# Kernel tuning notes

Measured on AMD Instinct MI355X. Metric: run time of the kernel, lower is better.

Reference implementation:

```python
import jax, jax.numpy as jnp
import numpy as np

B, T, D_IN = 2, 2048, 1024
H, D_HEAD = 16, 64
D_INNER = H * D_HEAD  # 1024
D_OUT = D_HEAD        # out_proj maps d_inner -> d_out


def setup_inputs() -> dict:
    key = jax.random.key(0)
    ks = jax.random.split(key, 6)
    s_in = 1.0 / np.sqrt(D_IN)
    s_inner = 1.0 / np.sqrt(D_INNER)
    return {
        "x": jax.random.normal(ks[0], (B, T, D_IN), dtype=jnp.float32),
        "Wq": jax.random.uniform(ks[1], (D_IN, D_INNER), jnp.float32, -s_in, s_in),
        "Wk": jax.random.uniform(ks[2], (D_IN, D_INNER), jnp.float32, -s_in, s_in),
        "Wv": jax.random.uniform(ks[3], (D_IN, D_INNER), jnp.float32, -s_in, s_in),
        "Wo": jax.random.uniform(ks[4], (D_INNER, D_OUT), jnp.float32, -s_inner, s_inner),
        "bo": jax.random.uniform(ks[5], (D_OUT,), jnp.float32, -s_inner, s_inner),
    }


def reference(x, Wq, Wk, Wv, Wo, bo):
    b, t, _ = x.shape
    # projections -> [b, h, t, d]
    def split_heads(y):
        return y.reshape(b, t, H, D_HEAD).transpose(0, 2, 1, 3)
    q = split_heads(x @ Wq)
    k = split_heads(x @ Wk)
    v = split_heads(x @ Wv)
    scores = jnp.einsum("bhqd,bhkd->bhqk", q, k)
    causal = jnp.triu(jnp.ones((t, t), dtype=bool), k=1)
    scores = jnp.where(causal, -jnp.inf, scores)
    # NOTE: original scales by sqrt(d_out*num_heads), not sqrt(head_dim)
    attn = jax.nn.softmax(scores / np.sqrt(D_INNER), axis=-1)
    y = jnp.einsum("bhqk,bhkd->bhqd", attn, v)
    y = y.transpose(0, 2, 1, 3).reshape(b, t, D_INNER)
    return y @ Wo + bo
```

## Files before the change

kernel.cpp:

```cpp
#include <hip/hip_runtime.h>

typedef __attribute__((ext_vector_type(8))) short short8;
typedef __attribute__((ext_vector_type(4))) float f32x4;
typedef __attribute__((ext_vector_type(8))) unsigned short ushort8v;


__device__ __forceinline__ unsigned short f2bf(float f) {
  union { float f; unsigned int u; } x; x.f = f;
  unsigned int r = x.u + 0x7FFFu + ((x.u >> 16) & 1u);
  return (unsigned short)(r >> 16);
}

__device__ __forceinline__ void gload_lds16(const void* g, void* l) {
  __builtin_amdgcn_global_load_lds(
      (const __attribute__((address_space(1))) void*)g,
      (__attribute__((address_space(3))) void*)l, 16, 0, 0);
}


__global__ __launch_bounds__(256) void prep(
    const float* __restrict__ x,
    const float* __restrict__ Wq, const float* __restrict__ Wk, const float* __restrict__ Wv,
    const float* __restrict__ Wo, const float* __restrict__ bo,
    unsigned short* __restrict__ xb,
    unsigned short* __restrict__ wqt, unsigned short* __restrict__ wkt,
    unsigned short* __restrict__ wvt, unsigned short* __restrict__ wot,
    float* __restrict__ out) {
  __shared__ float tile[32][33];
  int b = blockIdx.x;
  if (b < 4096) {
    int i = (b * 256 + threadIdx.x) * 4;
    float4 f = *(const float4*)(x + i);
    ushort4 o;
    o.x = f2bf(f.x); o.y = f2bf(f.y); o.z = f2bf(f.z); o.w = f2bf(f.w);
    *(ushort4*)(xb + i) = o;
  } else if (b < 7168) {
    int idx = b - 4096;
    int z = idx >> 10, rem = idx & 1023;
    const float* src = (z == 0) ? Wq : (z == 1) ? Wk : Wv;
    unsigned short* dst = (z == 0) ? wqt : (z == 1) ? wkt : wvt;
    int kx = (rem & 31) * 32, ny = (rem >> 5) * 32;
    int tx = threadIdx.x & 31, ty = threadIdx.x >> 5;
    #pragma unroll
    for (int r = 0; r < 32; r += 8)
      tile[ty + r][tx] = src[(size_t)(kx + ty + r) * 1024 + ny + tx];
    __syncthreads();
    #pragma unroll
    for (int r = 0; r < 32; r += 8)
      dst[(size_t)(ny + ty + r) * 1024 + kx + tx] = f2bf(tile[tx][ty + r]);
  } else if (b < 7232) {
    int idx = b - 7168;
    int kx = (idx & 31) * 32, ny = (idx >> 5) * 32;
    int tx = threadIdx.x & 31, ty = threadIdx.x >> 5;
    #pragma unroll
    for (int r = 0; r < 32; r += 8)
      tile[ty + r][tx] = Wo[(size_t)(kx + ty + r) * 64 + ny + tx];
    __syncthreads();
    #pragma unroll
    for (int r = 0; r < 32; r += 8)
      wot[(size_t)(ny + ty + r) * 1024 + kx + tx] = f2bf(tile[tx][ty + r]);
  } else {
    int t = (b - 7232) * 256 + threadIdx.x;
    float4 bi = *(const float4*)(bo + (t & 15) * 4);
    *(float4*)(out + (size_t)t * 4) = bi;
  }
}


__global__ __launch_bounds__(256) void qkv_gemm(
    const unsigned short* __restrict__ Xb,
    const unsigned short* __restrict__ Wqt, const unsigned short* __restrict__ Wkt,
    const unsigned short* __restrict__ Wvt,
    unsigned short* __restrict__ Oq, unsigned short* __restrict__ Ok,
    unsigned short* __restrict__ Ovt) {
  constexpr int Kd = 1024;
  __shared__ __align__(16) unsigned short As[128 * 64];
  __shared__ __align__(16) unsigned short Bs[128 * 64];
  int z = blockIdx.z;
  int m0, n0;
  const unsigned short *Arow, *Brow;
  if (z == 2) {
    m0 = blockIdx.y * 128; n0 = blockIdx.x * 128;
    Arow = Wvt; Brow = Xb;
  } else {
    m0 = blockIdx.x * 128; n0 = blockIdx.y * 128;
    Arow = Xb; Brow = (z == 0) ? Wqt : Wkt;
  }
  int tid = threadIdx.x, lane = tid & 63, wave = tid >> 6;
  int wm = wave >> 1, wn = wave & 1;
  int l15 = lane & 15, quad = lane >> 4;
  int swz = l15 & 7;

  f32x4 acc[4][4] = {};

  for (int k0 = 0; k0 < Kd; k0 += 64) {
    __syncthreads();
    #pragma unroll
    for (int r = 0; r < 4; ++r) {
      int i = tid + 256 * r;
      int row = i >> 3, c8 = i & 7;
      int gc8 = c8 ^ (row & 7);
      gload_lds16(Arow + (size_t)(m0 + row) * Kd + k0 + gc8 * 8, &As[i * 8]);
    }
    #pragma unroll
    for (int r = 0; r < 4; ++r) {
      int i = tid + 256 * r;
      int row = i >> 3, c8 = i & 7;
      int gc8 = c8 ^ (row & 7);
      gload_lds16(Brow + (size_t)(n0 + row) * Kd + k0 + gc8 * 8, &Bs[i * 8]);
    }
    __syncthreads();
    short8 af[4][2], bf[4][2];
    #pragma unroll
    for (int s = 0; s < 2; ++s) {
      #pragma unroll
      for (int i = 0; i < 4; ++i)
        af[i][s] = *(const short8*)&As[(wm * 64 + i * 16 + l15) * 64 + (((s << 2) + quad) ^ swz) * 8];
      #pragma unroll
      for (int j = 0; j < 4; ++j)
        bf[j][s] = *(const short8*)&Bs[(wn * 64 + j * 16 + l15) * 64 + (((s << 2) + quad) ^ swz) * 8];
    }
    #pragma unroll
    for (int s = 0; s < 2; ++s)
      #pragma unroll
      for (int i = 0; i < 4; ++i)
        #pragma unroll
        for (int j = 0; j < 4; ++j)
          acc[i][j] = __builtin_amdgcn_mfma_f32_16x16x32_bf16(af[i][s], bf[j][s], acc[i][j], 0, 0, 0);
  }

  if (z == 2) {
    #pragma unroll
    for (int i = 0; i < 4; ++i) {
      int dmbase = m0 + wm * 64 + i * 16 + quad * 4;
      #pragma unroll
      for (int j = 0; j < 4; ++j) {
        int tn = n0 + wn * 64 + j * 16 + l15;
        int b = tn >> 11, t = tn & 2047;
        #pragma unroll
        for (int r = 0; r < 4; ++r) {
          int dm = dmbase + r;
          int h = dm >> 6, d = dm & 63;
          Ovt[(((size_t)(b * 16 + h) * 64 + d) << 11) + t] = f2bf(acc[i][j][r]);
        }
      }
    }
  } else {
    unsigned short* O = (z == 0) ? Oq : Ok;
    float scale = (z == 0) ? 0.03125f : 1.0f;
    #pragma unroll
    for (int i = 0; i < 4; ++i) {
      int mbase = m0 + wm * 64 + i * 16 + quad * 4;
      #pragma unroll
      for (int j = 0; j < 4; ++j) {
        int n = n0 + wn * 64 + j * 16 + l15;
        int h = n >> 6, d = n & 63;
        #pragma unroll
        for (int r = 0; r < 4; ++r) {
          int mm = mbase + r;
          int b = mm >> 11, t = mm & 2047;
          size_t off = (((size_t)(b * 16 + h) * 2048 + t) << 6) + d;
          O[off] = f2bf(acc[i][j][r] * scale);
        }
      }
    }
  }
}


__global__ __launch_bounds__(256, 4) void attn4(
    const unsigned short* __restrict__ Qg, const unsigned short* __restrict__ Kg,
    const unsigned short* __restrict__ Vtg, unsigned short* __restrict__ Yg) {
  constexpr int T = 2048;
  __shared__ __align__(16) unsigned short Ks[64 * 72];
  __shared__ __align__(16) unsigned short Vs[64 * 72];
  __shared__ __align__(16) unsigned short Ps[4][16 * 72];
  int bh = blockIdx.y;
  int p = (blockIdx.x + blockIdx.y) & 15;
  int tid = threadIdx.x, lane = tid & 63, wave = tid >> 6;
  int l15 = lane & 15, quad = lane >> 4;
  const unsigned short* Qb = Qg + (size_t)bh * T * 64;
  const unsigned short* Kb = Kg + (size_t)bh * T * 64;
  const unsigned short* Vb = Vtg + (size_t)bh * 64 * T;
  int h = bh & 15, b = bh >> 4;

  for (int phase = 0; phase < 2; ++phase) {
    int qt = phase ? (31 - p) : p;
    int qw = qt * 64 + wave * 16;

    short8 qf[2];
    #pragma unroll
    for (int s = 0; s < 2; ++s)
      qf[s] = *(const short8*)(Qb + (size_t)(qw + l15) * 64 + quad * 8 + 32 * s);

    f32x4 Oacc[4] = {};
    float m_run = -__builtin_inff(), l_run = 0.f;

    ushort8v kpre[2], vpre[2];
    #pragma unroll
    for (int r = 0; r < 2; ++r) {
      int i = tid + 256 * r;
      kpre[r] = *(const ushort8v*)(Kb + (size_t)(i >> 3) * 64 + (i & 7) * 8);
      vpre[r] = *(const ushort8v*)(Vb + (size_t)(i >> 3) * T + (i & 7) * 8);
    }

    for (int kt = 0; kt <= qt; ++kt) {
      __syncthreads();
      #pragma unroll
      for (int r = 0; r < 2; ++r) {
        int i = tid + 256 * r;
        *(ushort8v*)&Ks[(i >> 3) * 72 + (i & 7) * 8] = kpre[r];
        *(ushort8v*)&Vs[(i >> 3) * 72 + (i & 7) * 8] = vpre[r];
      }
      __syncthreads();
      if (kt < qt) {
        #pragma unroll
        for (int r = 0; r < 2; ++r) {
          int i = tid + 256 * r;
          kpre[r] = *(const ushort8v*)(Kb + (size_t)((kt + 1) * 64 + (i >> 3)) * 64 + (i & 7) * 8);
          vpre[r] = *(const ushort8v*)(Vb + (size_t)(i >> 3) * T + (kt + 1) * 64 + (i & 7) * 8);
        }
      }

      f32x4 S[4] = {};
      #pragma unroll
      for (int s = 0; s < 2; ++s)
        #pragma unroll
        for (int mi = 0; mi < 4; ++mi) {
          short8 kf = *(const short8*)&Ks[(mi * 16 + l15) * 72 + quad * 8 + 32 * s];
          S[mi] = __builtin_amdgcn_mfma_f32_16x16x32_bf16(kf, qf[s], S[mi], 0, 0, 0);
        }

      if (kt == qt) {
        int ql = wave * 16 + l15;
        #pragma unroll
        for (int mi = 0; mi < 4; ++mi) {
          int tokl = mi * 16 + quad * 4;
          #pragma unroll
          for (int r = 0; r < 4; ++r)
            if (tokl + r > ql) S[mi][r] = -__builtin_inff();
        }
      }

      float vmax = -__builtin_inff();
      #pragma unroll
      for (int mi = 0; mi < 4; ++mi)
        #pragma unroll
        for (int r = 0; r < 4; ++r)
          vmax = fmaxf(vmax, S[mi][r]);
      vmax = fmaxf(vmax, __shfl_xor(vmax, 16));
      vmax = fmaxf(vmax, __shfl_xor(vmax, 32));
      float mnew = fmaxf(m_run, vmax);
      float alpha = __expf(m_run - mnew);
      m_run = mnew;
      float rs = 0.f;
      #pragma unroll
      for (int mi = 0; mi < 4; ++mi) {
        float p0 = __expf(S[mi][0] - mnew);
        float p1 = __expf(S[mi][1] - mnew);
        float p2 = __expf(S[mi][2] - mnew);
        float p3 = __expf(S[mi][3] - mnew);
        rs += (p0 + p1) + (p2 + p3);
        union { float f; unsigned int u; } a0{p0}, a1{p1}, a2{p2}, a3{p3};
        uint2 pk;
        pk.x = ((a0.u + 0x8000u) >> 16) | ((a1.u + 0x8000u) & 0xFFFF0000u);
        pk.y = ((a2.u + 0x8000u) >> 16) | ((a3.u + 0x8000u) & 0xFFFF0000u);
        *(uint2*)&Ps[wave][l15 * 72 + mi * 16 + quad * 4] = pk;
      }
      rs += __shfl_xor(rs, 16);
      rs += __shfl_xor(rs, 32);
      l_run = l_run * alpha + rs;

      #pragma unroll
      for (int r = 0; r < 4; ++r) {
        float a = __shfl(alpha, quad * 4 + r);
        #pragma unroll
        for (int jd = 0; jd < 4; ++jd)
          Oacc[jd][r] *= a;
      }

      #pragma unroll
      for (int s = 0; s < 2; ++s) {
        short8 pf = *(const short8*)&Ps[wave][l15 * 72 + quad * 8 + 32 * s];
        #pragma unroll
        for (int jd = 0; jd < 4; ++jd) {
          short8 vf = *(const short8*)&Vs[(jd * 16 + l15) * 72 + quad * 8 + 32 * s];
          Oacc[jd] = __builtin_amdgcn_mfma_f32_16x16x32_bf16(pf, vf, Oacc[jd], 0, 0, 0);
        }
      }
    }

    #pragma unroll
    for (int r = 0; r < 4; ++r) {
      float linv = 1.f / __shfl(l_run, quad * 4 + r);
      int q = qw + quad * 4 + r;
      size_t row = (size_t)(b * 2048 + q) * 1024 + h * 64;
      #pragma unroll
      for (int jd = 0; jd < 4; ++jd)
        Yg[row + jd * 16 + l15] = f2bf(Oacc[jd][r] * linv);
    }
  }
}


__global__ __launch_bounds__(256) void oproj(
    const unsigned short* __restrict__ Y, const unsigned short* __restrict__ Wot,
    float* __restrict__ out) {
  __shared__ __align__(16) unsigned short As[64 * 32];
  __shared__ __align__(16) unsigned short Bs[64 * 32];
  int m0 = blockIdx.x * 64;
  int kbase = blockIdx.y * 256;
  int tid = threadIdx.x, lane = tid & 63, wave = tid >> 6;
  int l15 = lane & 15, quad = lane >> 4;
  f32x4 acc[4] = {};
  for (int k0 = kbase; k0 < kbase + 256; k0 += 32) {
    __syncthreads();
    {
      int row = tid >> 2, c8 = (tid & 3) * 8;
      gload_lds16(Y + (size_t)(m0 + row) * 1024 + k0 + c8, &As[tid * 8]);
      gload_lds16(Wot + (size_t)row * 1024 + k0 + c8, &Bs[tid * 8]);
    }
    __syncthreads();
    short8 af = *(const short8*)&As[(wave * 16 + l15) * 32 + quad * 8];
    #pragma unroll
    for (int j = 0; j < 4; ++j) {
      short8 bf = *(const short8*)&Bs[(j * 16 + l15) * 32 + quad * 8];
      acc[j] = __builtin_amdgcn_mfma_f32_16x16x32_bf16(af, bf, acc[j], 0, 0, 0);
    }
  }
  #pragma unroll
  for (int j = 0; j < 4; ++j) {
    int n = j * 16 + l15;
    #pragma unroll
    for (int r = 0; r < 4; ++r) {
      int m = m0 + wave * 16 + quad * 4 + r;
      atomicAdd(&out[(size_t)m * 64 + n], acc[j][r]);
    }
  }
}


extern "C" void kernel_launch(void* const* d_in, const int* in_sizes, int n_in,
                              void* d_out, int out_size, void* d_ws, size_t ws_size,
                              hipStream_t stream) {
  const float* x  = (const float*)d_in[0];
  const float* Wq = (const float*)d_in[1];
  const float* Wk = (const float*)d_in[2];
  const float* Wv = (const float*)d_in[3];
  const float* Wo = (const float*)d_in[4];
  const float* bo = (const float*)d_in[5];
  float* out = (float*)d_out;
  char* ws = (char*)d_ws;

  unsigned short* xb  = (unsigned short*)(ws);
  unsigned short* wqt = (unsigned short*)(ws + (8ull << 20));
  unsigned short* wkt = (unsigned short*)(ws + (10ull << 20));
  unsigned short* wvt = (unsigned short*)(ws + (12ull << 20));
  unsigned short* wot = (unsigned short*)(ws + (14ull << 20));
  unsigned short* q   = (unsigned short*)(ws + (15ull << 20));
  unsigned short* k   = (unsigned short*)(ws + (23ull << 20));
  unsigned short* vt  = (unsigned short*)(ws + (31ull << 20));
  unsigned short* y   = (unsigned short*)(ws + (39ull << 20));

  prep<<<7488, 256, 0, stream>>>(x, Wq, Wk, Wv, Wo, bo, xb, wqt, wkt, wvt, wot, out);
  qkv_gemm<<<dim3(32, 8, 3), 256, 0, stream>>>(xb, wqt, wkt, wvt, q, k, vt);
  attn4<<<dim3(16, 32), 256, 0, stream>>>(q, k, vt, y);
  oproj<<<dim3(64, 4), 256, 0, stream>>>(y, wot, out);
}
```

Baseline: 177.0 us.

## Load V fragments directly from global and swap PV MFMA operand order

The attention kernel stops staging V tiles through shared memory. Each wave now loads its V^T fragments straight from global memory every key tile. The PV MFMA operands are swapped so the output accumulator is laid out with queries along lanes, which removes the per-row alpha and l shuffles and allows packed 8-byte bf16 output stores. This cuts LDS traffic and one shared buffer, but adds redundant global/L2 loads of V per wave with no prefetch, and launch bounds drop to 2 blocks per SIMD target.

```diff
diff --git a/kernel.cpp b/kernel.cpp
--- a/kernel.cpp
+++ b/kernel.cpp
@@ -168,15 +168,14 @@
 }
 
 
-__global__ __launch_bounds__(256, 4) void attn4(
+__global__ __launch_bounds__(256, 2) void attn6(
     const unsigned short* __restrict__ Qg, const unsigned short* __restrict__ Kg,
     const unsigned short* __restrict__ Vtg, unsigned short* __restrict__ Yg) {
   constexpr int T = 2048;
   __shared__ __align__(16) unsigned short Ks[64 * 72];
-  __shared__ __align__(16) unsigned short Vs[64 * 72];
   __shared__ __align__(16) unsigned short Ps[4][16 * 72];
   int bh = blockIdx.y;
-  int p = (blockIdx.x + blockIdx.y) & 15;
+  int pp = (blockIdx.x + blockIdx.y) & 15;
   int tid = threadIdx.x, lane = tid & 63, wave = tid >> 6;
   int l15 = lane & 15, quad = lane >> 4;
   const unsigned short* Qb = Qg + (size_t)bh * T * 64;
@@ -185,7 +184,7 @@
   int h = bh & 15, b = bh >> 4;
 
   for (int phase = 0; phase < 2; ++phase) {
-    int qt = phase ? (31 - p) : p;
+    int qt = phase ? (31 - pp) : pp;
     int qw = qt * 64 + wave * 16;
 
     short8 qf[2];
@@ -196,12 +195,11 @@
     f32x4 Oacc[4] = {};
     float m_run = -__builtin_inff(), l_run = 0.f;
 
-    ushort8v kpre[2], vpre[2];
+    ushort8v kpre[2];
     #pragma unroll
     for (int r = 0; r < 2; ++r) {
       int i = tid + 256 * r;
       kpre[r] = *(const ushort8v*)(Kb + (size_t)(i >> 3) * 64 + (i & 7) * 8);
-      vpre[r] = *(const ushort8v*)(Vb + (size_t)(i >> 3) * T + (i & 7) * 8);
     }
 
     for (int kt = 0; kt <= qt; ++kt) {
@@ -210,7 +208,6 @@
       for (int r = 0; r < 2; ++r) {
         int i = tid + 256 * r;
         *(ushort8v*)&Ks[(i >> 3) * 72 + (i & 7) * 8] = kpre[r];
-        *(ushort8v*)&Vs[(i >> 3) * 72 + (i & 7) * 8] = vpre[r];
       }
       __syncthreads();
       if (kt < qt) {
@@ -218,9 +215,14 @@
         for (int r = 0; r < 2; ++r) {
           int i = tid + 256 * r;
           kpre[r] = *(const ushort8v*)(Kb + (size_t)((kt + 1) * 64 + (i >> 3)) * 64 + (i & 7) * 8);
-          vpre[r] = *(const ushort8v*)(Vb + (size_t)(i >> 3) * T + (kt + 1) * 64 + (i & 7) * 8);
-        }
-      }
+        }
+      }
+      short8 vf[4][2];
+      #pragma unroll
+      for (int jd = 0; jd < 4; ++jd)
+        #pragma unroll
+        for (int s = 0; s < 2; ++s)
+          vf[jd][s] = *(const short8*)(Vb + (size_t)(jd * 16 + l15) * T + kt * 64 + s * 32 + quad * 8);
 
       f32x4 S[4] = {};
       #pragma unroll
@@ -272,32 +274,33 @@
       l_run = l_run * alpha + rs;
 
       #pragma unroll
-      for (int r = 0; r < 4; ++r) {
-        float a = __shfl(alpha, quad * 4 + r);
+      for (int jd = 0; jd < 4; ++jd)
+        #pragma unroll
+        for (int r = 0; r < 4; ++r)
+          Oacc[jd][r] *= alpha;
+
+      #pragma unroll
+      for (int s = 0; s < 2; ++s) {
+        short8 pf = *(const short8*)&Ps[wave][l15 * 72 + s * 32 + quad * 8];
         #pragma unroll
         for (int jd = 0; jd < 4; ++jd)
-          Oacc[jd][r] *= a;
-      }
-
-      #pragma unroll
-      for (int s = 0; s < 2; ++s) {
-        short8 pf = *(const short8*)&Ps[wave][l15 * 72 + quad * 8 + 32 * s];
-        #pragma unroll
-        for (int jd = 0; jd < 4; ++jd) {
-          short8 vf = *(const short8*)&Vs[(jd * 16 + l15) * 72 + quad * 8 + 32 * s];
-          Oacc[jd] = __builtin_amdgcn_mfma_f32_16x16x32_bf16(pf, vf, Oacc[jd], 0, 0, 0);
-        }
-      }
-    }
-
-    #pragma unroll
-    for (int r = 0; r < 4; ++r) {
-      float linv = 1.f / __shfl(l_run, quad * 4 + r);
-      int q = qw + quad * 4 + r;
-      size_t row = (size_t)(b * 2048 + q) * 1024 + h * 64;
-      #pragma unroll
-      for (int jd = 0; jd < 4; ++jd)
-        Yg[row + jd * 16 + l15] = f2bf(Oacc[jd][r] * linv);
+          Oacc[jd] = __builtin_amdgcn_mfma_f32_16x16x32_bf16(vf[jd][s], pf, Oacc[jd], 0, 0, 0);
+      }
+    }
+
+    float linv = 1.f / l_run;
+    int q = qw + l15;
+    size_t row = (size_t)(b * 2048 + q) * 1024 + h * 64 + quad * 4;
+    #pragma unroll
+    for (int jd = 0; jd < 4; ++jd) {
+      union { float f; unsigned int u; } a0{Oacc[jd][0] * linv}, a1{Oacc[jd][1] * linv},
+                                         a2{Oacc[jd][2] * linv}, a3{Oacc[jd][3] * linv};
+      uint2 pk;
+      pk.x = ((a0.u + 0x7FFFu + ((a0.u >> 16) & 1u)) >> 16) |
+             ((a1.u + 0x7FFFu + ((a1.u >> 16) & 1u)) & 0xFFFF0000u);
+      pk.y = ((a2.u + 0x7FFFu + ((a2.u >> 16) & 1u)) >> 16) |
+             ((a3.u + 0x7FFFu + ((a3.u >> 16) & 1u)) & 0xFFFF0000u);
+      *(uint2*)(Yg + row + jd * 16) = pk;
     }
   }
 }
@@ -364,6 +367,6 @@
 
   prep<<<7488, 256, 0, stream>>>(x, Wq, Wk, Wv, Wo, bo, xb, wqt, wkt, wvt, wot, out);
   qkv_gemm<<<dim3(32, 8, 3), 256, 0, stream>>>(xb, wqt, wkt, wvt, q, k, vt);
-  attn4<<<dim3(16, 32), 256, 0, stream>>>(q, k, vt, y);
+  attn6<<<dim3(16, 32), 256, 0, stream>>>(q, k, vt, y);
   oproj<<<dim3(64, 4), 256, 0, stream>>>(y, wot, out);
 }
```

New measurement: 197.9 us. 1.12x slower.
